# Kernel optimization log

Measured on AMD Instinct MI355X. Metric: run time of the kernel, lower is better.

The kernel has to match this reference:

```python
import jax, jax.numpy as jnp
import numpy as np

N_NODES = 50000
N_EDGES = 1600000
ATOM_F = 64
FP_SIZE = 2048
N_GRAPHS = 2000


def setup_inputs() -> dict:
    key = jax.random.key(0)
    ks = jax.random.split(key, 12)
    s = 1.0 / np.sqrt(ATOM_F)
    x = jax.random.normal(ks[0], (N_NODES, ATOM_F), dtype=jnp.float32)
    H1_w = jax.random.normal(ks[1], (ATOM_F, ATOM_F), dtype=jnp.float32) * s
    H1_b = jnp.zeros((ATOM_F,), dtype=jnp.float32)
    W1_w = jax.random.normal(ks[2], (FP_SIZE, ATOM_F), dtype=jnp.float32) * s
    W1_b = jnp.zeros((FP_SIZE,), dtype=jnp.float32)
    H2_w = jax.random.normal(ks[3], (ATOM_F, ATOM_F), dtype=jnp.float32) * s
    H2_b = jnp.zeros((ATOM_F,), dtype=jnp.float32)
    W2_w = jax.random.normal(ks[4], (FP_SIZE, ATOM_F), dtype=jnp.float32) * s
    W2_b = jnp.zeros((FP_SIZE,), dtype=jnp.float32)
    edge_index = jax.random.randint(ks[5], (2, N_EDGES), 0, N_NODES, dtype=jnp.int64)
    batch = jnp.sort(jax.random.randint(ks[6], (N_NODES,), 0, N_GRAPHS, dtype=jnp.int64))
    return {
        "x": x,
        "H1_w": H1_w, "H1_b": H1_b, "W1_w": W1_w, "W1_b": W1_b,
        "H2_w": H2_w, "H2_b": H2_b, "W2_w": W2_w, "W2_b": W2_b,
        "edge_index": edge_index,
        "batch": batch,
        "num_graphs": N_GRAPHS,
    }


def reference(x, H1_w, H1_b, W1_w, W1_b, H2_w, H2_b, W2_w, W2_b,
              edge_index, batch, num_graphs):
    n = x.shape[0]
    src, dst = edge_index[0], edge_index[1]

    def loop(h, Hw, Hb, Ww, Wb):
        # sum aggregation over incoming edges; '+ h' accounts for add_self_loops
        agg = jax.ops.segment_sum(h[src], dst, num_segments=n) + h
        upd = jax.nn.sigmoid(agg @ Hw.T + Hb)          # [N, atom_features]
        fp = jax.nn.softmax(upd @ Ww.T + Wb, axis=-1)  # [N, fp_size]
        return upd, fp

    h1, fp1 = loop(x, H1_w, H1_b, W1_w, W1_b)
    _, fp2 = loop(h1, H2_w, H2_b, W2_w, W2_b)
    fingerprint = fp1 + fp2
    # pool per-node fingerprints into per-graph fingerprints
    return jax.ops.segment_sum(fingerprint, batch, num_segments=num_graphs)
```

## Files before the change

### kernel.cpp

```cpp
#include <hip/hip_runtime.h>
#include <hip/hip_bf16.h>

#define AF 64
#define NFP 2048
#define GPB 2

typedef __attribute__((ext_vector_type(8))) short bf16x8;
typedef __attribute__((ext_vector_type(4))) float f32x4;

__device__ __forceinline__ ushort f2bf(float f) {
    unsigned u = __float_as_uint(f);
    return (ushort)((u + 0x7FFF + ((u >> 16) & 1)) >> 16);
}
__device__ __forceinline__ float bf2f(ushort u) {
    return __uint_as_float((unsigned)u << 16);
}

__global__ __launch_bounds__(256) void hist_kernel(
    const int* __restrict__ keys, int* __restrict__ counts, int n)
{
    int e = blockIdx.x * 256 + threadIdx.x;
    if (e < n) atomicAdd(&counts[keys[e]], 1);
}

__global__ __launch_bounds__(256) void hist_part_kernel(
    const int* __restrict__ dst, int* __restrict__ counts,
    int n_edges, int npr, int nchunks)
{
    int r = blockIdx.x & 7;
    int c = blockIdx.x >> 3;
    int lo = r * npr, hi = lo + npr;
    int per = (n_edges + nchunks - 1) / nchunks;
    int e0 = c * per;
    int e1 = e0 + per; if (e1 > n_edges) e1 = n_edges;
    for (int e = e0 + (int)threadIdx.x; e < e1; e += 256) {
        int d = dst[e];
        if (d >= lo && d < hi) atomicAdd(&counts[d], 1);
    }
}

__global__ __launch_bounds__(1024) void scan_kernel(int* data, int n)
{
    __shared__ int wsum[16];
    __shared__ int chunk_total;
    int t = threadIdx.x, lane = t & 63, w = t >> 6;
    int running = 0;
    for (int base = 0; base < n; base += 1024) {
        int i = base + t;
        int v = (i < n) ? data[i] : 0;
        int x = v;
        #pragma unroll
        for (int off = 1; off < 64; off <<= 1) {
            int y = __shfl_up(x, off);
            if (lane >= off) x += y;
        }
        if (lane == 63) wsum[w] = x;
        __syncthreads();
        if (t == 0) {
            int s = 0;
            #pragma unroll
            for (int q = 0; q < 16; ++q) { int tmp = wsum[q]; wsum[q] = s; s += tmp; }
            chunk_total = s;
        }
        __syncthreads();
        if (i < n) data[i] = x - v + wsum[w] + running;
        running += chunk_total;
        __syncthreads();
    }
    if (t == 0) data[n] = running;
}

__global__ __launch_bounds__(256) void scatter_part_kernel(
    const int* __restrict__ src, const int* __restrict__ dst,
    int* __restrict__ cursor, int* __restrict__ esrc,
    int n_edges, int npr, int nchunks)
{
    int r = blockIdx.x & 7;
    int c = blockIdx.x >> 3;
    int lo = r * npr, hi = lo + npr;
    int per = (n_edges + nchunks - 1) / nchunks;
    int e0 = c * per;
    int e1 = e0 + per; if (e1 > n_edges) e1 = n_edges;
    for (int e = e0 + (int)threadIdx.x; e < e1; e += 256) {
        int d = dst[e];
        if (d >= lo && d < hi) {
            int pos = atomicAdd(&cursor[d], 1);
            esrc[pos] = src[e];
        }
    }
}

__global__ __launch_bounds__(256) void f2bf_kernel(
    const float* __restrict__ W, ushort* __restrict__ Wbf, int n)
{
    int i = blockIdx.x * 256 + threadIdx.x;
    if (i < n) Wbf[i] = f2bf(W[i]);
}

__global__ __launch_bounds__(256) void agg_mlp_kernel(
    const ushort* __restrict__ hbf, const int* __restrict__ offsets,
    const int* __restrict__ esrc, const float* __restrict__ Hw,
    const float* __restrict__ Hb, ushort* __restrict__ outbf, int n_nodes)
{
    __shared__ float Hw_s[AF * 65];
    __shared__ __align__(16) float part[4][8][AF];
    __shared__ float a_red[4][AF];
    __shared__ float hb_s[AF];

    int t = threadIdx.x;
    for (int idx = t; idx < AF * AF; idx += 256) {
        int j = idx >> 6, k = idx & 63;
        Hw_s[j * 65 + k] = Hw[idx];
    }
    if (t < AF) hb_s[t] = Hb[t];

    int w = t >> 6, lane = t & 63;
    int sub = lane >> 3, f8 = lane & 7;
    int i = blockIdx.x * 4 + w;

    float acc[8] = {0.f, 0.f, 0.f, 0.f, 0.f, 0.f, 0.f, 0.f};
    if (i < n_nodes) {
        int o0 = offsets[i], o1 = offsets[i + 1];
        const int* ep = esrc + o0;
        int deg = o1 - o0;
        for (int j = 0; j < deg; j += 8) {
            int jj = j + sub;
            if (jj < deg) {
                int s = ep[jj];
                bf16x8 v = *(const bf16x8*)(hbf + (size_t)s * AF + f8 * 8);
                #pragma unroll
                for (int q = 0; q < 8; ++q) acc[q] += bf2f((ushort)v[q]);
            }
        }
    }
    *(float4*)&part[w][sub][f8 * 8]     = make_float4(acc[0], acc[1], acc[2], acc[3]);
    *(float4*)&part[w][sub][f8 * 8 + 4] = make_float4(acc[4], acc[5], acc[6], acc[7]);
    __syncthreads();

    if (i < n_nodes) {
        float val = bf2f(hbf[(size_t)i * AF + lane]);
        #pragma unroll
        for (int s8 = 0; s8 < 8; ++s8) val += part[w][s8][lane];
        a_red[w][lane] = val;
    }
    __syncthreads();

    if (i < n_nodes) {
        float z = hb_s[lane];
        #pragma unroll
        for (int k = 0; k < AF; ++k)
            z = fmaf(a_red[w][k], Hw_s[lane * 65 + k], z);
        float sg = 1.f / (1.f + __expf(-z));
        outbf[(size_t)i * AF + lane] = f2bf(sg);
    }
}

__global__ __launch_bounds__(256) void denom_kernel(
    const ushort* __restrict__ updbf, const ushort* __restrict__ Wbf,
    const float* __restrict__ Wb, float* __restrict__ sden, int n_nodes)
{
    __shared__ float red[4][32];

    int t = threadIdx.x, wave = t >> 6, lane = t & 63;
    int G = lane >> 4, sl = lane & 15;
    int cw = wave * 512;
    int base = blockIdx.x * 32;

    bf16x8 a00, a01, a10, a11;
    {
        const ushort* p0 = updbf + (size_t)(base + sl) * AF + G * 8;
        a00 = *(const bf16x8*)p0;
        a01 = *(const bf16x8*)(p0 + 32);
        const ushort* p1 = updbf + (size_t)(base + 16 + sl) * AF + G * 8;
        a10 = *(const bf16x8*)p1;
        a11 = *(const bf16x8*)(p1 + 32);
    }
    float s0[4] = {0.f, 0.f, 0.f, 0.f};
    float s1[4] = {0.f, 0.f, 0.f, 0.f};

    const ushort* wp0 = Wbf + (size_t)(cw + sl) * AF + G * 8;
    bf16x8 nb0 = *(const bf16x8*)wp0;
    bf16x8 nb1 = *(const bf16x8*)(wp0 + 32);

    #pragma unroll 4
    for (int ct = 0; ct < 32; ++ct) {
        bf16x8 b0 = nb0, b1 = nb1;
        if (ct < 31) {
            const ushort* wp = Wbf + (size_t)(cw + (ct + 1) * 16 + sl) * AF + G * 8;
            nb0 = *(const bf16x8*)wp;
            nb1 = *(const bf16x8*)(wp + 32);
        }
        float bias = Wb[cw + ct * 16 + sl];
        f32x4 d0 = {0.f, 0.f, 0.f, 0.f};
        d0 = __builtin_amdgcn_mfma_f32_16x16x32_bf16(a00, b0, d0, 0, 0, 0);
        d0 = __builtin_amdgcn_mfma_f32_16x16x32_bf16(a01, b1, d0, 0, 0, 0);
        f32x4 d1 = {0.f, 0.f, 0.f, 0.f};
        d1 = __builtin_amdgcn_mfma_f32_16x16x32_bf16(a10, b0, d1, 0, 0, 0);
        d1 = __builtin_amdgcn_mfma_f32_16x16x32_bf16(a11, b1, d1, 0, 0, 0);
        #pragma unroll
        for (int r = 0; r < 4; ++r) {
            s0[r] += __expf(d0[r] + bias);
            s1[r] += __expf(d1[r] + bias);
        }
    }
    #pragma unroll
    for (int mask = 1; mask <= 8; mask <<= 1) {
        #pragma unroll
        for (int r = 0; r < 4; ++r) {
            s0[r] += __shfl_xor(s0[r], mask);
            s1[r] += __shfl_xor(s1[r], mask);
        }
    }
    if (sl == 0) {
        #pragma unroll
        for (int r = 0; r < 4; ++r) {
            red[wave][G * 4 + r]      = s0[r];
            red[wave][16 + G * 4 + r] = s1[r];
        }
    }
    __syncthreads();
    if (t < 32) {
        float s = red[0][t] + red[1][t] + red[2][t] + red[3][t];
        int n = base + t;
        if (n < n_nodes) sden[n] = 1.f / s;
    }
}

template <int ACCUM>
__global__ __launch_bounds__(512) void fp_pool_graph_kernel(
    const ushort* __restrict__ updbf, const ushort* __restrict__ Wbf,
    const float* __restrict__ Wb, const float* __restrict__ sden,
    const int* __restrict__ goff, float* __restrict__ out, int n_graphs)
{
    __shared__ __align__(16) float facc[NFP];
    __shared__ __align__(16) float wb_s[NFP];

    int t = threadIdx.x, wave = t >> 6, lane = t & 63;
    int G = lane >> 4, sl = lane & 15;
    int c0 = wave * 256;

    *(float4*)&wb_s[c0 + lane * 4] = *(const float4*)&Wb[c0 + lane * 4];

    int g0 = blockIdx.x * GPB;
    int g1 = g0 + GPB; if (g1 > n_graphs) g1 = n_graphs;

    for (int g = g0; g < g1; ++g) {
        *(float4*)&facc[c0 + lane * 4] = make_float4(0.f, 0.f, 0.f, 0.f);
        int gs = goff[g], ge = goff[g + 1];

        for (int i0 = gs; i0 < ge; i0 += 32) {
            bf16x8 a00, a01, a10, a11;
            {
                const ushort* p0 = updbf + (size_t)(i0 + sl) * AF + G * 8;
                a00 = *(const bf16x8*)p0;
                a01 = *(const bf16x8*)(p0 + 32);
                const ushort* p1 = updbf + (size_t)(i0 + 16 + sl) * AF + G * 8;
                a10 = *(const bf16x8*)p1;
                a11 = *(const bf16x8*)(p1 + 32);
            }
            float sc0[4], sc1[4];
            #pragma unroll
            for (int r = 0; r < 4; ++r) {
                int n0 = i0 + G * 4 + r;
                sc0[r] = (n0 < ge) ? sden[n0] : 0.f;
                int n1 = n0 + 16;
                sc1[r] = (n1 < ge) ? sden[n1] : 0.f;
            }

            const ushort* wp0 = Wbf + (size_t)(c0 + sl) * AF + G * 8;
            bf16x8 nb0 = *(const bf16x8*)wp0;
            bf16x8 nb1 = *(const bf16x8*)(wp0 + 32);

            #pragma unroll
            for (int ct = 0; ct < 16; ++ct) {
                bf16x8 b0 = nb0, b1 = nb1;
                if (ct < 15) {
                    const ushort* wp = Wbf + (size_t)(c0 + (ct + 1) * 16 + sl) * AF + G * 8;
                    nb0 = *(const bf16x8*)wp;
                    nb1 = *(const bf16x8*)(wp + 32);
                }
                int col = c0 + ct * 16 + sl;
                float bias = wb_s[col];
                f32x4 d0 = {0.f, 0.f, 0.f, 0.f};
                d0 = __builtin_amdgcn_mfma_f32_16x16x32_bf16(a00, b0, d0, 0, 0, 0);
                d0 = __builtin_amdgcn_mfma_f32_16x16x32_bf16(a01, b1, d0, 0, 0, 0);
                f32x4 d1 = {0.f, 0.f, 0.f, 0.f};
                d1 = __builtin_amdgcn_mfma_f32_16x16x32_bf16(a10, b0, d1, 0, 0, 0);
                d1 = __builtin_amdgcn_mfma_f32_16x16x32_bf16(a11, b1, d1, 0, 0, 0);
                float c = 0.f;
                #pragma unroll
                for (int r = 0; r < 4; ++r) {
                    c += __expf(d0[r] + bias) * sc0[r];
                    c += __expf(d1[r] + bias) * sc1[r];
                }
                c += __shfl_xor(c, 16);
                c += __shfl_xor(c, 32);
                if (G == 0) facc[col] += c;
            }
        }

        float4 fa = *(float4*)&facc[c0 + lane * 4];
        float* po = &out[(size_t)g * NFP];
        if (ACCUM) {
            float4 oa = *(const float4*)&po[c0 + lane * 4];
            fa.x += oa.x; fa.y += oa.y; fa.z += oa.z; fa.w += oa.w;
        }
        *(float4*)&po[c0 + lane * 4] = fa;
    }
}

extern "C" void kernel_launch(void* const* d_in, const int* in_sizes, int n_in,
                              void* d_out, int out_size, void* d_ws, size_t ws_size,
                              hipStream_t stream)
{
    const float* x    = (const float*)d_in[0];
    const float* H1_w = (const float*)d_in[1];
    const float* H1_b = (const float*)d_in[2];
    const float* W1_w = (const float*)d_in[3];
    const float* W1_b = (const float*)d_in[4];
    const float* H2_w = (const float*)d_in[5];
    const float* H2_b = (const float*)d_in[6];
    const float* W2_w = (const float*)d_in[7];
    const float* W2_b = (const float*)d_in[8];
    const int*   ei   = (const int*)d_in[9];
    const int*   batch= (const int*)d_in[10];

    const int n_nodes  = in_sizes[0] / AF;
    const int n_edges  = in_sizes[9] / 2;
    const int n_graphs = out_size / NFP;
    const int npad     = ((n_nodes + 127) / 128) * 128;
    const int* src = ei;
    const int* dst = ei + n_edges;
    float* out = (float*)d_out;

    ushort* xbf     = (ushort*)d_ws;
    ushort* ubf1    = xbf  + (size_t)npad * AF;
    ushort* ubf2    = ubf1 + (size_t)npad * AF;
    ushort* Wbf1    = ubf2 + (size_t)npad * AF;
    ushort* Wbf2    = Wbf1 + (size_t)NFP * AF;
    float*  sden    = (float*)(Wbf2 + (size_t)NFP * AF);
    int*    offsets = (int*)(sden + npad);
    int*    cursor  = offsets + (n_nodes + 1);
    int*    goff    = cursor + (n_nodes + 1);
    int*    esrc    = goff + (n_graphs + 1);

    const int nb = (n_nodes + 255) / 256;
    const int mlp_blocks = (n_nodes + 3) / 4;
    const int dn_blocks  = npad / 32;
    const int fp_blocks  = (n_graphs + GPB - 1) / GPB;
    const int wn = NFP * AF;
    const int xn = n_nodes * AF;
    const int npr = (n_nodes + 7) / 8;
    const int nchunks = 256;

    f2bf_kernel<<<(xn + 255) / 256, 256, 0, stream>>>(x, xbf, xn);
    f2bf_kernel<<<(wn + 255) / 256, 256, 0, stream>>>(W1_w, Wbf1, wn);
    f2bf_kernel<<<(wn + 255) / 256, 256, 0, stream>>>(W2_w, Wbf2, wn);
    hipMemsetAsync(xbf + (size_t)n_nodes * AF, 0,
                   (size_t)(npad - n_nodes) * AF * sizeof(ushort), stream);
    hipMemsetAsync(ubf1 + (size_t)n_nodes * AF, 0,
                   (size_t)(npad - n_nodes) * AF * sizeof(ushort), stream);
    hipMemsetAsync(ubf2 + (size_t)n_nodes * AF, 0,
                   (size_t)(npad - n_nodes) * AF * sizeof(ushort), stream);
    hipMemsetAsync(offsets, 0, (size_t)(n_nodes + 1) * sizeof(int), stream);
    hipMemsetAsync(goff, 0, (size_t)(n_graphs + 1) * sizeof(int), stream);
    hist_part_kernel<<<nchunks * 8, 256, 0, stream>>>(dst, offsets, n_edges, npr, nchunks);
    hist_kernel<<<nb, 256, 0, stream>>>(batch, goff, n_nodes);
    scan_kernel<<<1, 1024, 0, stream>>>(offsets, n_nodes);
    scan_kernel<<<1, 1024, 0, stream>>>(goff, n_graphs);
    hipMemcpyAsync(cursor, offsets, (size_t)n_nodes * sizeof(int),
                   hipMemcpyDeviceToDevice, stream);
    scatter_part_kernel<<<nchunks * 8, 256, 0, stream>>>(src, dst, cursor, esrc,
                                                         n_edges, npr, nchunks);

    agg_mlp_kernel<<<mlp_blocks, 256, 0, stream>>>(xbf, offsets, esrc,
                                                   H1_w, H1_b, ubf1, n_nodes);
    denom_kernel<<<dn_blocks, 256, 0, stream>>>(ubf1, Wbf1, W1_b, sden, n_nodes);
    fp_pool_graph_kernel<0><<<fp_blocks, 512, 0, stream>>>(ubf1, Wbf1, W1_b,
                                                           sden, goff, out, n_graphs);

    agg_mlp_kernel<<<mlp_blocks, 256, 0, stream>>>(ubf1, offsets, esrc,
                                                   H2_w, H2_b, ubf2, n_nodes);
    denom_kernel<<<dn_blocks, 256, 0, stream>>>(ubf2, Wbf2, W2_b, sden, n_nodes);
    fp_pool_graph_kernel<1><<<fp_blocks, 512, 0, stream>>>(ubf2, Wbf2, W2_b,
                                                           sden, goff, out, n_graphs);
}
```

Before: 676.3 us.

## Fuse softmax denominator and fingerprint pooling into node-tiled kernel with partial reduce

Replaces the separate denominator kernel and the graph-tiled pooling kernel with one kernel per 32-node tile. It computes the softmax denominators, then recomputes the logits and pools them per graph into shared-memory partial rows. A small reduce kernel then sums the partials per graph into the output. This removes the sden round trip and the load imbalance of graph-sized tiles, at the cost of an extra partial buffer write/read, a per-graph masked loop, and a 32KB shared array that may limit occupancy.

```diff
diff --git a/kernel.cpp b/kernel.cpp
--- a/kernel.cpp
+++ b/kernel.cpp
@@ -3,7 +3,7 @@
 
 #define AF 64
 #define NFP 2048
-#define GPB 2
+#define MAXG 4
 
 typedef __attribute__((ext_vector_type(8))) short bf16x8;
 typedef __attribute__((ext_vector_type(4))) float f32x4;
@@ -155,52 +155,58 @@
     }
 }
 
-__global__ __launch_bounds__(256) void denom_kernel(
+__global__ __launch_bounds__(256) void fp_node_pool_kernel(
     const ushort* __restrict__ updbf, const ushort* __restrict__ Wbf,
-    const float* __restrict__ Wb, float* __restrict__ sden, int n_nodes)
+    const float* __restrict__ Wb, const int* __restrict__ batch,
+    float* __restrict__ partial, float* __restrict__ out, int n_nodes)
 {
     __shared__ float red[4][32];
+    __shared__ float sden_s[32];
+    __shared__ int   bat_s[32];
+    __shared__ __align__(16) float pacc[MAXG][NFP];
 
     int t = threadIdx.x, wave = t >> 6, lane = t & 63;
     int G = lane >> 4, sl = lane & 15;
     int cw = wave * 512;
-    int base = blockIdx.x * 32;
+    int b = blockIdx.x;
+    int i0 = b * 32;
 
     bf16x8 a00, a01, a10, a11;
     {
-        const ushort* p0 = updbf + (size_t)(base + sl) * AF + G * 8;
+        const ushort* p0 = updbf + (size_t)(i0 + sl) * AF + G * 8;
         a00 = *(const bf16x8*)p0;
         a01 = *(const bf16x8*)(p0 + 32);
-        const ushort* p1 = updbf + (size_t)(base + 16 + sl) * AF + G * 8;
+        const ushort* p1 = updbf + (size_t)(i0 + 16 + sl) * AF + G * 8;
         a10 = *(const bf16x8*)p1;
         a11 = *(const bf16x8*)(p1 + 32);
     }
+
     float s0[4] = {0.f, 0.f, 0.f, 0.f};
     float s1[4] = {0.f, 0.f, 0.f, 0.f};
-
-    const ushort* wp0 = Wbf + (size_t)(cw + sl) * AF + G * 8;
-    bf16x8 nb0 = *(const bf16x8*)wp0;
-    bf16x8 nb1 = *(const bf16x8*)(wp0 + 32);
-
-    #pragma unroll 4
-    for (int ct = 0; ct < 32; ++ct) {
-        bf16x8 b0 = nb0, b1 = nb1;
-        if (ct < 31) {
-            const ushort* wp = Wbf + (size_t)(cw + (ct + 1) * 16 + sl) * AF + G * 8;
-            nb0 = *(const bf16x8*)wp;
-            nb1 = *(const bf16x8*)(wp + 32);
-        }
-        float bias = Wb[cw + ct * 16 + sl];
-        f32x4 d0 = {0.f, 0.f, 0.f, 0.f};
-        d0 = __builtin_amdgcn_mfma_f32_16x16x32_bf16(a00, b0, d0, 0, 0, 0);
-        d0 = __builtin_amdgcn_mfma_f32_16x16x32_bf16(a01, b1, d0, 0, 0, 0);
-        f32x4 d1 = {0.f, 0.f, 0.f, 0.f};
-        d1 = __builtin_amdgcn_mfma_f32_16x16x32_bf16(a10, b0, d1, 0, 0, 0);
-        d1 = __builtin_amdgcn_mfma_f32_16x16x32_bf16(a11, b1, d1, 0, 0, 0);
-        #pragma unroll
-        for (int r = 0; r < 4; ++r) {
-            s0[r] += __expf(d0[r] + bias);
-            s1[r] += __expf(d1[r] + bias);
+    {
+        const ushort* wp0 = Wbf + (size_t)(cw + sl) * AF + G * 8;
+        bf16x8 nb0 = *(const bf16x8*)wp0;
+        bf16x8 nb1 = *(const bf16x8*)(wp0 + 32);
+        #pragma unroll 4
+        for (int ct = 0; ct < 32; ++ct) {
+            bf16x8 b0 = nb0, b1 = nb1;
+            if (ct < 31) {
+                const ushort* wp = Wbf + (size_t)(cw + (ct + 1) * 16 + sl) * AF + G * 8;
+                nb0 = *(const bf16x8*)wp;
+                nb1 = *(const bf16x8*)(wp + 32);
+            }
+            float bias = Wb[cw + ct * 16 + sl];
+            f32x4 d0 = {0.f, 0.f, 0.f, 0.f};
+            d0 = __builtin_amdgcn_mfma_f32_16x16x32_bf16(a00, b0, d0, 0, 0, 0);
+            d0 = __builtin_amdgcn_mfma_f32_16x16x32_bf16(a01, b1, d0, 0, 0, 0);
+            f32x4 d1 = {0.f, 0.f, 0.f, 0.f};
+            d1 = __builtin_amdgcn_mfma_f32_16x16x32_bf16(a10, b0, d1, 0, 0, 0);
+            d1 = __builtin_amdgcn_mfma_f32_16x16x32_bf16(a11, b1, d1, 0, 0, 0);
+            #pragma unroll
+            for (int r = 0; r < 4; ++r) {
+                s0[r] += __expf(d0[r] + bias);
+                s1[r] += __expf(d1[r] + bias);
+            }
         }
     }
     #pragma unroll
@@ -218,95 +224,118 @@
             red[wave][16 + G * 4 + r] = s1[r];
         }
     }
+    if (t < 32) {
+        int n = i0 + t;
+        bat_s[t] = batch[n < n_nodes ? n : (n_nodes - 1)];
+    }
     __syncthreads();
     if (t < 32) {
         float s = red[0][t] + red[1][t] + red[2][t] + red[3][t];
-        int n = base + t;
-        if (n < n_nodes) sden[n] = 1.f / s;
-    }
-}
-
-template <int ACCUM>
-__global__ __launch_bounds__(512) void fp_pool_graph_kernel(
-    const ushort* __restrict__ updbf, const ushort* __restrict__ Wbf,
-    const float* __restrict__ Wb, const float* __restrict__ sden,
-    const int* __restrict__ goff, float* __restrict__ out, int n_graphs)
-{
-    __shared__ __align__(16) float facc[NFP];
-    __shared__ __align__(16) float wb_s[NFP];
-
-    int t = threadIdx.x, wave = t >> 6, lane = t & 63;
-    int G = lane >> 4, sl = lane & 15;
-    int c0 = wave * 256;
-
-    *(float4*)&wb_s[c0 + lane * 4] = *(const float4*)&Wb[c0 + lane * 4];
-
-    int g0 = blockIdx.x * GPB;
-    int g1 = g0 + GPB; if (g1 > n_graphs) g1 = n_graphs;
-
-    for (int g = g0; g < g1; ++g) {
-        *(float4*)&facc[c0 + lane * 4] = make_float4(0.f, 0.f, 0.f, 0.f);
-        int gs = goff[g], ge = goff[g + 1];
-
-        for (int i0 = gs; i0 < ge; i0 += 32) {
-            bf16x8 a00, a01, a10, a11;
-            {
-                const ushort* p0 = updbf + (size_t)(i0 + sl) * AF + G * 8;
-                a00 = *(const bf16x8*)p0;
-                a01 = *(const bf16x8*)(p0 + 32);
-                const ushort* p1 = updbf + (size_t)(i0 + 16 + sl) * AF + G * 8;
-                a10 = *(const bf16x8*)p1;
-                a11 = *(const bf16x8*)(p1 + 32);
-            }
-            float sc0[4], sc1[4];
+        sden_s[t] = 1.f / s;
+    }
+    __syncthreads();
+
+    int g_first = bat_s[0];
+    int ng = bat_s[31] - g_first + 1;
+    int ngl = ng < MAXG ? ng : MAXG;
+
+    for (int gi = 0; gi < ngl; ++gi) {
+        *(float4*)&pacc[gi][cw + lane * 8]     = make_float4(0.f, 0.f, 0.f, 0.f);
+        *(float4*)&pacc[gi][cw + lane * 8 + 4] = make_float4(0.f, 0.f, 0.f, 0.f);
+    }
+
+    float sc0[4], sc1[4];
+    int gl0[4], gl1[4];
+    #pragma unroll
+    for (int r = 0; r < 4; ++r) {
+        int l0 = G * 4 + r, l1 = l0 + 16;
+        sc0[r] = (i0 + l0 < n_nodes) ? sden_s[l0] : 0.f;
+        sc1[r] = (i0 + l1 < n_nodes) ? sden_s[l1] : 0.f;
+        gl0[r] = bat_s[l0];
+        gl1[r] = bat_s[l1];
+    }
+
+    {
+        const ushort* wp0 = Wbf + (size_t)(cw + sl) * AF + G * 8;
+        bf16x8 nb0 = *(const bf16x8*)wp0;
+        bf16x8 nb1 = *(const bf16x8*)(wp0 + 32);
+        #pragma unroll 4
+        for (int ct = 0; ct < 32; ++ct) {
+            bf16x8 b0 = nb0, b1 = nb1;
+            if (ct < 31) {
+                const ushort* wp = Wbf + (size_t)(cw + (ct + 1) * 16 + sl) * AF + G * 8;
+                nb0 = *(const bf16x8*)wp;
+                nb1 = *(const bf16x8*)(wp + 32);
+            }
+            int col = cw + ct * 16 + sl;
+            float bias = Wb[col];
+            f32x4 d0 = {0.f, 0.f, 0.f, 0.f};
+            d0 = __builtin_amdgcn_mfma_f32_16x16x32_bf16(a00, b0, d0, 0, 0, 0);
+            d0 = __builtin_amdgcn_mfma_f32_16x16x32_bf16(a01, b1, d0, 0, 0, 0);
+            f32x4 d1 = {0.f, 0.f, 0.f, 0.f};
+            d1 = __builtin_amdgcn_mfma_f32_16x16x32_bf16(a10, b0, d1, 0, 0, 0);
+            d1 = __builtin_amdgcn_mfma_f32_16x16x32_bf16(a11, b1, d1, 0, 0, 0);
+            float e0[4], e1[4];
             #pragma unroll
             for (int r = 0; r < 4; ++r) {
-                int n0 = i0 + G * 4 + r;
-                sc0[r] = (n0 < ge) ? sden[n0] : 0.f;
-                int n1 = n0 + 16;
-                sc1[r] = (n1 < ge) ? sden[n1] : 0.f;
-            }
-
-            const ushort* wp0 = Wbf + (size_t)(c0 + sl) * AF + G * 8;
-            bf16x8 nb0 = *(const bf16x8*)wp0;
-            bf16x8 nb1 = *(const bf16x8*)(wp0 + 32);
-
-            #pragma unroll
-            for (int ct = 0; ct < 16; ++ct) {
-                bf16x8 b0 = nb0, b1 = nb1;
-                if (ct < 15) {
-                    const ushort* wp = Wbf + (size_t)(c0 + (ct + 1) * 16 + sl) * AF + G * 8;
-                    nb0 = *(const bf16x8*)wp;
-                    nb1 = *(const bf16x8*)(wp + 32);
-                }
-                int col = c0 + ct * 16 + sl;
-                float bias = wb_s[col];
-                f32x4 d0 = {0.f, 0.f, 0.f, 0.f};
-                d0 = __builtin_amdgcn_mfma_f32_16x16x32_bf16(a00, b0, d0, 0, 0, 0);
-                d0 = __builtin_amdgcn_mfma_f32_16x16x32_bf16(a01, b1, d0, 0, 0, 0);
-                f32x4 d1 = {0.f, 0.f, 0.f, 0.f};
-                d1 = __builtin_amdgcn_mfma_f32_16x16x32_bf16(a10, b0, d1, 0, 0, 0);
-                d1 = __builtin_amdgcn_mfma_f32_16x16x32_bf16(a11, b1, d1, 0, 0, 0);
+                e0[r] = __expf(d0[r] + bias) * sc0[r];
+                e1[r] = __expf(d1[r] + bias) * sc1[r];
+            }
+            for (int gi = 0; gi < ng; ++gi) {
+                int g = g_first + gi;
                 float c = 0.f;
                 #pragma unroll
                 for (int r = 0; r < 4; ++r) {
-                    c += __expf(d0[r] + bias) * sc0[r];
-                    c += __expf(d1[r] + bias) * sc1[r];
+                    c += (gl0[r] == g) ? e0[r] : 0.f;
+                    c += (gl1[r] == g) ? e1[r] : 0.f;
                 }
                 c += __shfl_xor(c, 16);
                 c += __shfl_xor(c, 32);
-                if (G == 0) facc[col] += c;
-            }
-        }
-
-        float4 fa = *(float4*)&facc[c0 + lane * 4];
-        float* po = &out[(size_t)g * NFP];
-        if (ACCUM) {
-            float4 oa = *(const float4*)&po[c0 + lane * 4];
-            fa.x += oa.x; fa.y += oa.y; fa.z += oa.z; fa.w += oa.w;
-        }
-        *(float4*)&po[c0 + lane * 4] = fa;
-    }
+                if (gi < MAXG) {
+                    if (G == 0) pacc[gi][col] += c;
+                } else if (G == 0) {
+                    unsafeAtomicAdd(&out[(size_t)g * NFP + col], c);
+                }
+            }
+        }
+    }
+
+    for (int gi = 0; gi < ng; ++gi) {
+        float* row = partial + (size_t)(b + g_first + gi) * NFP;
+        if (gi < MAXG) {
+            *(float4*)&row[cw + lane * 8]     = *(float4*)&pacc[gi][cw + lane * 8];
+            *(float4*)&row[cw + lane * 8 + 4] = *(float4*)&pacc[gi][cw + lane * 8 + 4];
+        } else {
+            *(float4*)&row[cw + lane * 8]     = make_float4(0.f, 0.f, 0.f, 0.f);
+            *(float4*)&row[cw + lane * 8 + 4] = make_float4(0.f, 0.f, 0.f, 0.f);
+        }
+    }
+}
+
+__global__ __launch_bounds__(256) void fp_reduce_kernel(
+    const float* __restrict__ partial, const int* __restrict__ goff,
+    float* __restrict__ out)
+{
+    int g = blockIdx.x, t = threadIdx.x;
+    int gs = goff[g], ge = goff[g + 1];
+    if (ge <= gs) return;
+    int b0 = gs >> 5, b1 = (ge - 1) >> 5;
+    float4 acc0 = make_float4(0.f, 0.f, 0.f, 0.f);
+    float4 acc1 = make_float4(0.f, 0.f, 0.f, 0.f);
+    for (int b = b0; b <= b1; ++b) {
+        const float* row = partial + (size_t)(b + g) * NFP;
+        float4 v0 = *(const float4*)&row[t * 8];
+        float4 v1 = *(const float4*)&row[t * 8 + 4];
+        acc0.x += v0.x; acc0.y += v0.y; acc0.z += v0.z; acc0.w += v0.w;
+        acc1.x += v1.x; acc1.y += v1.y; acc1.z += v1.z; acc1.w += v1.w;
+    }
+    float* po = &out[(size_t)g * NFP];
+    float4 o0 = *(float4*)&po[t * 8];
+    float4 o1 = *(float4*)&po[t * 8 + 4];
+    o0.x += acc0.x; o0.y += acc0.y; o0.z += acc0.z; o0.w += acc0.w;
+    o1.x += acc1.x; o1.y += acc1.y; o1.z += acc1.z; o1.w += acc1.w;
+    *(float4*)&po[t * 8]     = o0;
+    *(float4*)&po[t * 8 + 4] = o1;
 }
 
 extern "C" void kernel_launch(void* const* d_in, const int* in_sizes, int n_in,
@@ -333,21 +362,22 @@
     const int* dst = ei + n_edges;
     float* out = (float*)d_out;
 
+    const int fp_blocks = (n_nodes + 31) / 32;
+    const int npairs    = fp_blocks + n_graphs + 1;
+
     ushort* xbf     = (ushort*)d_ws;
     ushort* ubf1    = xbf  + (size_t)npad * AF;
     ushort* ubf2    = ubf1 + (size_t)npad * AF;
     ushort* Wbf1    = ubf2 + (size_t)npad * AF;
     ushort* Wbf2    = Wbf1 + (size_t)NFP * AF;
-    float*  sden    = (float*)(Wbf2 + (size_t)NFP * AF);
-    int*    offsets = (int*)(sden + npad);
+    float*  partial = (float*)(Wbf2 + (size_t)NFP * AF);
+    int*    offsets = (int*)(partial + (size_t)npairs * NFP);
     int*    cursor  = offsets + (n_nodes + 1);
     int*    goff    = cursor + (n_nodes + 1);
     int*    esrc    = goff + (n_graphs + 1);
 
     const int nb = (n_nodes + 255) / 256;
     const int mlp_blocks = (n_nodes + 3) / 4;
-    const int dn_blocks  = npad / 32;
-    const int fp_blocks  = (n_graphs + GPB - 1) / GPB;
     const int wn = NFP * AF;
     const int xn = n_nodes * AF;
     const int npr = (n_nodes + 7) / 8;
@@ -356,6 +386,7 @@
     f2bf_kernel<<<(xn + 255) / 256, 256, 0, stream>>>(x, xbf, xn);
     f2bf_kernel<<<(wn + 255) / 256, 256, 0, stream>>>(W1_w, Wbf1, wn);
     f2bf_kernel<<<(wn + 255) / 256, 256, 0, stream>>>(W2_w, Wbf2, wn);
+    hipMemsetAsync(out, 0, (size_t)out_size * sizeof(float), stream);
     hipMemsetAsync(xbf + (size_t)n_nodes * AF, 0,
                    (size_t)(npad - n_nodes) * AF * sizeof(ushort), stream);
     hipMemsetAsync(ubf1 + (size_t)n_nodes * AF, 0,
@@ -375,13 +406,13 @@
 
     agg_mlp_kernel<<<mlp_blocks, 256, 0, stream>>>(xbf, offsets, esrc,
                                                    H1_w, H1_b, ubf1, n_nodes);
-    denom_kernel<<<dn_blocks, 256, 0, stream>>>(ubf1, Wbf1, W1_b, sden, n_nodes);
-    fp_pool_graph_kernel<0><<<fp_blocks, 512, 0, stream>>>(ubf1, Wbf1, W1_b,
-                                                           sden, goff, out, n_graphs);
+    fp_node_pool_kernel<<<fp_blocks, 256, 0, stream>>>(ubf1, Wbf1, W1_b, batch,
+                                                       partial, out, n_nodes);
+    fp_reduce_kernel<<<n_graphs, 256, 0, stream>>>(partial, goff, out);
 
     agg_mlp_kernel<<<mlp_blocks, 256, 0, stream>>>(ubf1, offsets, esrc,
                                                    H2_w, H2_b, ubf2, n_nodes);
-    denom_kernel<<<dn_blocks, 256, 0, stream>>>(ubf2, Wbf2, W2_b, sden, n_nodes);
-    fp_pool_graph_kernel<1><<<fp_blocks, 512, 0, stream>>>(ubf2, Wbf2, W2_b,
-                                                           sden, goff, out, n_graphs);
-}
+    fp_node_pool_kernel<<<fp_blocks, 256, 0, stream>>>(ubf2, Wbf2, W2_b, batch,
+                                                       partial, out, n_nodes);
+    fp_reduce_kernel<<<n_graphs, 256, 0, stream>>>(partial, goff, out);
+}
```

New measurement: 647.7 us. -4.2%, faster.
